# Performance work log

Hardware: AMD Instinct MI355X
Metric: run time of the kernel (lower is better)

## Reference

```python
import jax, jax.numpy as jnp
import numpy as np

NEG_SLOPE = 0.2

def gat_conv(x, src, dst, W, a_src, a_dst, bias, N):
    # PyG GATConv, heads=1: h = xW; e_ij = LeakyReLU(a_src.h_j + a_dst.h_i)
    h = x @ W                                   # [N, H]
    as_ = h @ a_src                             # [N]
    ad_ = h @ a_dst                             # [N]
    e = jax.nn.leaky_relu(as_[src] + ad_[dst], NEG_SLOPE)   # [E]
    m = jax.ops.segment_max(e, dst, num_segments=N)          # per-target max
    w = jnp.exp(e - m[dst])
    denom = jax.ops.segment_sum(w, dst, num_segments=N)
    alpha = w / (denom[dst] + 1e-16)                          # [E]
    out = jax.ops.segment_sum(alpha[:, None] * h[src], dst, num_segments=N)
    return out + bias


def setup_inputs() -> dict:
    key = jax.random.key(0)
    N, E, D, H, A = 20000, 320000, 256, 256, 8
    ks = jax.random.split(key, 16)
    s = lambda k, shp, fan: jax.random.normal(k, shp, jnp.float32) * (1.0 / np.sqrt(fan))
    return {
        "obs": jax.random.normal(ks[0], (N, D), jnp.float32),
        "edge_index": jax.random.randint(ks[1], (2, E), 0, N, dtype=jnp.int32),
        "W1": s(ks[2], (D, H), D), "a1_src": s(ks[3], (H,), H), "a1_dst": s(ks[4], (H,), H), "b1": jnp.zeros((H,), jnp.float32),
        "W2": s(ks[5], (H, H), H), "a2_src": s(ks[6], (H,), H), "a2_dst": s(ks[7], (H,), H), "b2": jnp.zeros((H,), jnp.float32),
        "Wm1": s(ks[8], (H, H), H), "bm1": jnp.zeros((H,), jnp.float32),
        "Wm2": s(ks[9], (H, A), H), "bm2": jnp.zeros((A,), jnp.float32),
    }


def reference(obs, edge_index, W1, a1_src, a1_dst, b1, W2, a2_src, a2_dst, b2, Wm1, bm1, Wm2, bm2):
    N = obs.shape[0]
    loops = jnp.arange(N, dtype=edge_index.dtype)
    src = jnp.concatenate([edge_index[0], loops])   # add self-loops (PyG default)
    dst = jnp.concatenate([edge_index[1], loops])
    x = jax.nn.relu(gat_conv(obs, src, dst, W1, a1_src, a1_dst, b1, N))
    x = jax.nn.relu(gat_conv(x,   src, dst, W2, a2_src, a2_dst, b2, N))
    x = jax.nn.relu(x @ Wm1 + bm1)
    return jnp.tanh(x @ Wm2 + bm2)
```

## Files before the change

kernel.cpp:

```cpp
#include <hip/hip_runtime.h>
#include <hip/hip_bf16.h>
#include <math.h>
#include <stdio.h>

typedef __attribute__((ext_vector_type(8))) short short8;
typedef __attribute__((ext_vector_type(4))) float f32x4;
typedef __attribute__((ext_vector_type(4))) unsigned short us4;

__device__ __forceinline__ float us2f(unsigned short u) {
    return __uint_as_float(((unsigned)u) << 16);
}
__device__ __forceinline__ unsigned short f2us_rtn(float f) {
    return (unsigned short)__bfloat16_as_ushort(__float2bfloat16(f));
}

__global__ void prep_all(const float* __restrict__ Wa, const float* __restrict__ Wb,
                         const float* __restrict__ Wc,
                         unsigned short* __restrict__ TA, unsigned short* __restrict__ TB,
                         unsigned short* __restrict__ TC,
                         const float* __restrict__ X, unsigned short* __restrict__ Xb,
                         float* __restrict__ as1, float* __restrict__ ad1,
                         float* __restrict__ as2, float* __restrict__ ad2,
                         int* __restrict__ deg,
                         int K, int Nn, int N, int tot8) {
    const int tot = K * Nn;
    int idx = blockIdx.x * blockDim.x + threadIdx.x;
    if (idx < 3 * tot) {
        const float* W;
        unsigned short* T;
        if (idx < tot) { W = Wa; T = TA; }
        else if (idx < 2 * tot) { W = Wb; T = TB; idx -= tot; }
        else { W = Wc; T = TC; idx -= 2 * tot; }
        const int n = idx / K, k = idx - n * K;
        T[idx] = f2us_rtn(W[(size_t)k * Nn + n]);
        return;
    }
    idx -= 3 * tot;
    if (idx < 5 * N) {
        if (idx < N) as1[idx] = 0.f;
        else if (idx < 2 * N) ad1[idx - N] = 0.f;
        else if (idx < 3 * N) as2[idx - 2 * N] = 0.f;
        else if (idx < 4 * N) ad2[idx - 3 * N] = 0.f;
        else deg[idx - 4 * N] = 0;
        return;
    }
    idx -= 5 * N;
    if (idx < tot8) {
        const float4 a = *(const float4*)(X + (size_t)idx * 8);
        const float4 b = *(const float4*)(X + (size_t)idx * 8 + 4);
        short8 o;
        const float f[8] = {a.x, a.y, a.z, a.w, b.x, b.y, b.z, b.w};
#pragma unroll
        for (int e = 0; e < 8; e++) o[e] = (short)f2us_rtn(f[e]);
        *(short8*)(Xb + (size_t)idx * 8) = o;
    }
}

#define LP 72
__global__ __launch_bounds__(256) void gemm_mfma(const unsigned short* __restrict__ A,
                                                 const unsigned short* __restrict__ Bt,
                                                 const float* __restrict__ avs,
                                                 const float* __restrict__ avd,
                                                 float* __restrict__ as_,
                                                 float* __restrict__ ad_,
                                                 unsigned short* __restrict__ C,
                                                 int M, int Nn, int K) {
    __shared__ unsigned short sA[64 * LP];
    __shared__ unsigned short sB[128 * LP];
    const int tid = threadIdx.x;
    const int wave = tid >> 6, lane = tid & 63;
    const int m16 = lane & 15, quad = lane >> 4;
    const int row0 = blockIdx.x * 64, col0 = blockIdx.y * 128;
    const int wr = (wave >> 1) * 32, wc = (wave & 1) * 64;
    const int ar = tid >> 2, akc = (tid & 3) * 8;
    const int bkc = (tid & 7) * 8, bcb = tid >> 3;

    f32x4 acc[2][4] = {};
    for (int k0 = 0; k0 < K; k0 += 64) {
        {
            const int gr = (row0 + ar) < M ? (row0 + ar) : (M - 1);
            const unsigned short* Ap = A + (size_t)gr * K + k0 + akc;
            *(short8*)&sA[ar * LP + akc]      = *(const short8*)Ap;
            *(short8*)&sA[ar * LP + akc + 32] = *(const short8*)(Ap + 32);
        }
#pragma unroll
        for (int q = 0; q < 4; q++) {
            const int colq = bcb + 32 * q;
            *(short8*)&sB[colq * LP + bkc] =
                *(const short8*)(Bt + (size_t)(col0 + colq) * K + k0 + bkc);
        }
        __syncthreads();
#pragma unroll
        for (int ks = 0; ks < 2; ks++) {
            short8 ah[2];
#pragma unroll
            for (int mi = 0; mi < 2; mi++)
                ah[mi] = *(const short8*)&sA[(wr + mi * 16 + m16) * LP + ks * 32 + quad * 8];
#pragma unroll
            for (int ni = 0; ni < 4; ni++) {
                const short8 bv = *(const short8*)&sB[(wc + ni * 16 + m16) * LP + ks * 32 + quad * 8];
#pragma unroll
                for (int mi = 0; mi < 2; mi++)
                    acc[mi][ni] = __builtin_amdgcn_mfma_f32_16x16x32_bf16(ah[mi], bv, acc[mi][ni], 0, 0, 0);
            }
        }
        __syncthreads();
    }
    float ps[2][4] = {}, pd[2][4] = {};
#pragma unroll
    for (int mi = 0; mi < 2; mi++) {
        const int orow_base = row0 + wr + mi * 16 + quad * 4;
#pragma unroll
        for (int ni = 0; ni < 4; ni++) {
            const int ocol = col0 + wc + ni * 16 + m16;
            const float asv = avs[ocol], adv = avd[ocol];
#pragma unroll
            for (int r = 0; r < 4; r++) {
                const int orow = orow_base + r;
                if (orow < M) {
                    const float v = acc[mi][ni][r];
                    C[(size_t)orow * Nn + ocol] = f2us_rtn(v);
                    ps[mi][r] = fmaf(v, asv, ps[mi][r]);
                    pd[mi][r] = fmaf(v, adv, pd[mi][r]);
                }
            }
        }
    }
#pragma unroll
    for (int mi = 0; mi < 2; mi++)
#pragma unroll
        for (int r = 0; r < 4; r++)
#pragma unroll
            for (int off = 1; off < 16; off <<= 1) {
                ps[mi][r] += __shfl_xor(ps[mi][r], off);
                pd[mi][r] += __shfl_xor(pd[mi][r], off);
            }
    if (m16 == 0) {
#pragma unroll
        for (int mi = 0; mi < 2; mi++) {
            const int orow_base = row0 + wr + mi * 16 + quad * 4;
#pragma unroll
            for (int r = 0; r < 4; r++) {
                const int orow = orow_base + r;
                if (orow < M) {
                    atomicAdd(&as_[orow], ps[mi][r]);
                    atomicAdd(&ad_[orow], pd[mi][r]);
                }
            }
        }
    }
}

__global__ __launch_bounds__(256) void gemm_head(const unsigned short* __restrict__ A,
                                                 const unsigned short* __restrict__ Bt,
                                                 const float* __restrict__ bias1,
                                                 const float* __restrict__ W2,
                                                 const float* __restrict__ bias2,
                                                 float* __restrict__ out,
                                                 int M, int K, int Aout) {
    __shared__ unsigned short sA[64 * LP];
    __shared__ unsigned short sB[256 * LP];
    __shared__ float pLDS[2][64][8];
    const int tid = threadIdx.x;
    const int wave = tid >> 6, lane = tid & 63;
    const int m16 = lane & 15, quad = lane >> 4;
    const int row0 = blockIdx.x * 64;
    const int wr = (wave >> 1) * 32, wc = (wave & 1) * 128;
    const int ar = tid >> 2, akc = (tid & 3) * 8;
    const int bkc = (tid & 7) * 8, bcb = tid >> 3;

    f32x4 acc[2][8] = {};
    for (int k0 = 0; k0 < K; k0 += 64) {
        {
            const int gr = (row0 + ar) < M ? (row0 + ar) : (M - 1);
            const unsigned short* Ap = A + (size_t)gr * K + k0 + akc;
            *(short8*)&sA[ar * LP + akc]      = *(const short8*)Ap;
            *(short8*)&sA[ar * LP + akc + 32] = *(const short8*)(Ap + 32);
        }
#pragma unroll
        for (int q = 0; q < 8; q++) {
            const int colq = bcb + 32 * q;
            *(short8*)&sB[colq * LP + bkc] =
                *(const short8*)(Bt + (size_t)colq * K + k0 + bkc);
        }
        __syncthreads();
#pragma unroll
        for (int ks = 0; ks < 2; ks++) {
            short8 ah[2];
#pragma unroll
            for (int mi = 0; mi < 2; mi++)
                ah[mi] = *(const short8*)&sA[(wr + mi * 16 + m16) * LP + ks * 32 + quad * 8];
#pragma unroll
            for (int ni = 0; ni < 8; ni++) {
                const short8 bv = *(const short8*)&sB[(wc + ni * 16 + m16) * LP + ks * 32 + quad * 8];
#pragma unroll
                for (int mi = 0; mi < 2; mi++)
                    acc[mi][ni] = __builtin_amdgcn_mfma_f32_16x16x32_bf16(ah[mi], bv, acc[mi][ni], 0, 0, 0);
            }
        }
        __syncthreads();
    }
    float p[2][4][8] = {};
#pragma unroll
    for (int ni = 0; ni < 8; ni++) {
        const int ocol = wc + ni * 16 + m16;
        const float b1v = bias1[ocol];
        float w2[8];
#pragma unroll
        for (int a = 0; a < 8; a++) w2[a] = W2[ocol * 8 + a];
#pragma unroll
        for (int mi = 0; mi < 2; mi++)
#pragma unroll
            for (int r = 0; r < 4; r++) {
                const float v = fmaxf(acc[mi][ni][r] + b1v, 0.f);
#pragma unroll
                for (int a = 0; a < 8; a++) p[mi][r][a] = fmaf(v, w2[a], p[mi][r][a]);
            }
    }
#pragma unroll
    for (int off = 1; off < 16; off <<= 1)
#pragma unroll
        for (int mi = 0; mi < 2; mi++)
#pragma unroll
            for (int r = 0; r < 4; r++)
#pragma unroll
                for (int a = 0; a < 8; a++) p[mi][r][a] += __shfl_xor(p[mi][r][a], off);
    if (m16 == 0) {
        const int half = wc >> 7;
#pragma unroll
        for (int mi = 0; mi < 2; mi++) {
            const int lrow = wr + mi * 16 + quad * 4;
#pragma unroll
            for (int r = 0; r < 4; r++)
#pragma unroll
                for (int a = 0; a < 8; a++) pLDS[half][lrow + r][a] = p[mi][r][a];
        }
    }
    __syncthreads();
#pragma unroll
    for (int u = 0; u < 2; u++) {
        const int idx = tid * 2 + u;
        const int lrow = idx >> 3, a = idx & 7;
        const int orow = row0 + lrow;
        if (orow < M && a < Aout)
            out[(size_t)orow * Aout + a] =
                tanhf(pLDS[0][lrow][a] + pLDS[1][lrow][a] + bias2[a]);
    }
}
#undef LP

__global__ void count_kernel(const int* __restrict__ dstA, int* __restrict__ deg, int E, int Etot) {
    const int e = blockIdx.x * blockDim.x + threadIdx.x;
    if (e >= Etot) return;
    const int d = (e < E) ? dstA[e] : (e - E);
    atomicAdd(&deg[d], 1);
}

__global__ __launch_bounds__(1024) void scan_kernel(const int* __restrict__ deg,
                                                    int* __restrict__ offs,
                                                    int* __restrict__ cursor, int N) {
    __shared__ int sums[1024];
    const int t = threadIdx.x;
    const int chunk = (N + 1023) / 1024;
    const int start = t * chunk;
    int s = 0;
    for (int i = 0; i < chunk; i++) {
        const int p = start + i;
        if (p < N) s += deg[p];
    }
    sums[t] = s;
    __syncthreads();
    for (int off = 1; off < 1024; off <<= 1) {
        const int add = (t >= off) ? sums[t - off] : 0;
        __syncthreads();
        sums[t] += add;
        __syncthreads();
    }
    int run = (t > 0) ? sums[t - 1] : 0;
    for (int i = 0; i < chunk; i++) {
        const int p = start + i;
        if (p < N) { offs[p] = run; cursor[p] = run; run += deg[p]; }
    }
    if (t == 0) offs[N] = sums[1023];
}

__global__ void scatter_kernel(const int* __restrict__ srcA, const int* __restrict__ dstA,
                               int* __restrict__ cursor, int* __restrict__ esrc, int E, int Etot) {
    const int e = blockIdx.x * blockDim.x + threadIdx.x;
    if (e >= Etot) return;
    int s, d;
    if (e < E) { s = srcA[e]; d = dstA[e]; } else { s = d = e - E; }
    const int slot = atomicAdd(&cursor[d], 1);
    esrc[slot] = s;
}

__global__ __launch_bounds__(256) void agg_kernel(const unsigned short* __restrict__ hb,
                                                  const int* __restrict__ offs,
                                                  const int* __restrict__ esrc,
                                                  const float* __restrict__ as_,
                                                  const float* __restrict__ ad_,
                                                  const float* __restrict__ bias,
                                                  unsigned short* __restrict__ xout, int N) {
    const int n = blockIdx.x * 4 + (threadIdx.x >> 6);
    if (n >= N) return;
    const int lane = threadIdx.x & 63;
    const int f0 = lane * 4;
    const int b = offs[n], e2 = offs[n + 1];
    const float adn = ad_[n];
    float a0 = 0.f, a1 = 0.f, a2 = 0.f, a3 = 0.f, wsum = 0.f;
    int j = b;
    for (; j + 8 <= e2; j += 8) {
        int s[8];
#pragma unroll
        for (int u = 0; u < 8; u++) s[u] = esrc[j + u];
        us4 pv[8];
#pragma unroll
        for (int u = 0; u < 8; u++) pv[u] = *(const us4*)(hb + (size_t)s[u] * 256 + f0);
        float w[8];
#pragma unroll
        for (int u = 0; u < 8; u++) {
            float v = as_[s[u]] + adn;
            v = v > 0.f ? v : 0.2f * v;
            w[u] = __expf(v);
        }
#pragma unroll
        for (int u = 0; u < 8; u++) {
            a0 = fmaf(w[u], us2f(pv[u][0]), a0);
            a1 = fmaf(w[u], us2f(pv[u][1]), a1);
            a2 = fmaf(w[u], us2f(pv[u][2]), a2);
            a3 = fmaf(w[u], us2f(pv[u][3]), a3);
            wsum += w[u];
        }
    }
    for (; j < e2; j++) {
        const int s = esrc[j];
        float v = as_[s] + adn;
        v = v > 0.f ? v : 0.2f * v;
        const float w = __expf(v);
        const us4 pv = *(const us4*)(hb + (size_t)s * 256 + f0);
        a0 = fmaf(w, us2f(pv[0]), a0);
        a1 = fmaf(w, us2f(pv[1]), a1);
        a2 = fmaf(w, us2f(pv[2]), a2);
        a3 = fmaf(w, us2f(pv[3]), a3);
        wsum += w;
    }
    const float inv = 1.0f / (wsum + 1e-16f);
    float r0 = fmaxf(a0 * inv + bias[f0], 0.f);
    float r1 = fmaxf(a1 * inv + bias[f0 + 1], 0.f);
    float r2 = fmaxf(a2 * inv + bias[f0 + 2], 0.f);
    float r3 = fmaxf(a3 * inv + bias[f0 + 3], 0.f);
    us4 o;
    o[0] = f2us_rtn(r0); o[1] = f2us_rtn(r1); o[2] = f2us_rtn(r2); o[3] = f2us_rtn(r3);
    *(us4*)(xout + (size_t)n * 256 + f0) = o;
}

extern "C" void kernel_launch(void* const* d_in, const int* in_sizes, int n_in,
                              void* d_out, int out_size, void* d_ws, size_t ws_size,
                              hipStream_t stream) {
    const float* obs = (const float*)d_in[0];
    const int* eidx  = (const int*)d_in[1];
    const float* W1  = (const float*)d_in[2];
    const float* a1s = (const float*)d_in[3];
    const float* a1d = (const float*)d_in[4];
    const float* b1  = (const float*)d_in[5];
    const float* W2  = (const float*)d_in[6];
    const float* a2s = (const float*)d_in[7];
    const float* a2d = (const float*)d_in[8];
    const float* b2v = (const float*)d_in[9];
    const float* Wm1 = (const float*)d_in[10];
    const float* bm1 = (const float*)d_in[11];
    const float* Wm2 = (const float*)d_in[12];
    const float* bm2 = (const float*)d_in[13];
    float* out = (float*)d_out;

    const int Hh = in_sizes[3];
    const int Dd = in_sizes[2] / Hh;
    const int N  = in_sizes[0] / Dd;
    const int E  = in_sizes[1] / 2;
    const int Etot = E + N;
    const int Aout = in_sizes[12] / Hh;

    const int* srcA = eidx;
    const int* dstA = eidx + E;

    size_t off = 0;
    char* ws = (char*)d_ws;
    auto alloc = [&](size_t bytes) -> char* {
        char* p = ws + off;
        off = (off + bytes + 15) & ~(size_t)15;
        return p;
    };
    unsigned short* obs_b = (unsigned short*)alloc((size_t)N * Dd * 2);
    unsigned short* h     = (unsigned short*)alloc((size_t)N * Hh * 2);
    unsigned short* xb    = (unsigned short*)alloc((size_t)N * Hh * 2);
    float* as1   = (float*)alloc((size_t)N * 4);
    float* ad1   = (float*)alloc((size_t)N * 4);
    float* as2   = (float*)alloc((size_t)N * 4);
    float* ad2   = (float*)alloc((size_t)N * 4);
    int* deg     = (int*)alloc((size_t)N * 4);
    int* offs    = (int*)alloc((size_t)(N + 1) * 4);
    int* cursor  = (int*)alloc((size_t)N * 4);
    int* esrc    = (int*)alloc((size_t)Etot * 4);
    const size_t wsz = (size_t)Dd * Hh;
    unsigned short* W1t = (unsigned short*)alloc(wsz * 2);
    unsigned short* W2t = (unsigned short*)alloc(wsz * 2);
    unsigned short* Wmt = (unsigned short*)alloc(wsz * 2);

    const int eb = 256;
    const int eg = (Etot + eb - 1) / eb;
    const dim3 ggrid((N + 63) / 64, Hh / 128);
    const int nrow = (N + 63) / 64;

    const int tot8 = (N * Dd) / 8;
    const int ptot = 3 * (int)wsz + 5 * N + tot8;
    prep_all<<<(ptot + 255) / 256, 256, 0, stream>>>(
        W1, W2, Wm1, W1t, W2t, Wmt, obs, obs_b, as1, ad1, as2, ad2, deg, Dd, Hh, N, tot8);

    count_kernel<<<eg, eb, 0, stream>>>(dstA, deg, E, Etot);
    scan_kernel<<<1, 1024, 0, stream>>>(deg, offs, cursor, N);
    scatter_kernel<<<eg, eb, 0, stream>>>(srcA, dstA, cursor, esrc, E, Etot);

    gemm_mfma<<<ggrid, 256, 0, stream>>>(obs_b, W1t, a1s, a1d, as1, ad1, h, N, Hh, Dd);
    agg_kernel<<<(N + 3) / 4, 256, 0, stream>>>(h, offs, esrc, as1, ad1, b1, xb, N);

    gemm_mfma<<<ggrid, 256, 0, stream>>>(xb, W2t, a2s, a2d, as2, ad2, h, N, Hh, Hh);
    agg_kernel<<<(N + 3) / 4, 256, 0, stream>>>(h, offs, esrc, as2, ad2, b2v, xb, N);

    gemm_head<<<nrow, 256, 0, stream>>>(xb, Wmt, bm1, Wm2, bm2, out, N, Hh, Aout);
}
```

Measured before the change: 266.0 us.

## Fuse fp32-to-bf16 obs conversion into GEMM load and split aggregation by feature slice

The first GEMM now reads fp32 obs directly and converts it to bf16 while staging into shared memory. This removes the separate conversion pass in prep_all and the bf16 copy of obs it wrote to the workspace. The aggregation kernel is also split so that each block handles one 64-feature slice of four nodes, with each lane reading a single bf16 element instead of four. That gives four times more blocks for parallelism, but recomputes the edge weights four times and issues narrower gathers.

```diff
diff --git a/kernel.cpp b/kernel.cpp
--- a/kernel.cpp
+++ b/kernel.cpp
@@ -14,15 +14,27 @@
     return (unsigned short)__bfloat16_as_ushort(__float2bfloat16(f));
 }
 
+__device__ __forceinline__ void stage8(const unsigned short* Ap, unsigned short* dst) {
+    *(short8*)dst = *(const short8*)Ap;
+}
+__device__ __forceinline__ void stage8(const float* Ap, unsigned short* dst) {
+    const float4 a = *(const float4*)Ap;
+    const float4 b = *(const float4*)(Ap + 4);
+    const float f[8] = {a.x, a.y, a.z, a.w, b.x, b.y, b.z, b.w};
+    short8 o;
+#pragma unroll
+    for (int e = 0; e < 8; e++) o[e] = (short)f2us_rtn(f[e]);
+    *(short8*)dst = o;
+}
+
 __global__ void prep_all(const float* __restrict__ Wa, const float* __restrict__ Wb,
                          const float* __restrict__ Wc,
                          unsigned short* __restrict__ TA, unsigned short* __restrict__ TB,
                          unsigned short* __restrict__ TC,
-                         const float* __restrict__ X, unsigned short* __restrict__ Xb,
                          float* __restrict__ as1, float* __restrict__ ad1,
                          float* __restrict__ as2, float* __restrict__ ad2,
                          int* __restrict__ deg,
-                         int K, int Nn, int N, int tot8) {
+                         int K, int Nn, int N) {
     const int tot = K * Nn;
     int idx = blockIdx.x * blockDim.x + threadIdx.x;
     if (idx < 3 * tot) {
@@ -42,22 +54,12 @@
         else if (idx < 3 * N) as2[idx - 2 * N] = 0.f;
         else if (idx < 4 * N) ad2[idx - 3 * N] = 0.f;
         else deg[idx - 4 * N] = 0;
-        return;
-    }
-    idx -= 5 * N;
-    if (idx < tot8) {
-        const float4 a = *(const float4*)(X + (size_t)idx * 8);
-        const float4 b = *(const float4*)(X + (size_t)idx * 8 + 4);
-        short8 o;
-        const float f[8] = {a.x, a.y, a.z, a.w, b.x, b.y, b.z, b.w};
-#pragma unroll
-        for (int e = 0; e < 8; e++) o[e] = (short)f2us_rtn(f[e]);
-        *(short8*)(Xb + (size_t)idx * 8) = o;
     }
 }
 
 #define LP 72
-__global__ __launch_bounds__(256) void gemm_mfma(const unsigned short* __restrict__ A,
+template <typename TA>
+__global__ __launch_bounds__(256) void gemm_mfma(const TA* __restrict__ A,
                                                  const unsigned short* __restrict__ Bt,
                                                  const float* __restrict__ avs,
                                                  const float* __restrict__ avd,
@@ -79,9 +81,9 @@
     for (int k0 = 0; k0 < K; k0 += 64) {
         {
             const int gr = (row0 + ar) < M ? (row0 + ar) : (M - 1);
-            const unsigned short* Ap = A + (size_t)gr * K + k0 + akc;
-            *(short8*)&sA[ar * LP + akc]      = *(const short8*)Ap;
-            *(short8*)&sA[ar * LP + akc + 32] = *(const short8*)(Ap + 32);
+            const TA* Ap = A + (size_t)gr * K + k0 + akc;
+            stage8(Ap,      &sA[ar * LP + akc]);
+            stage8(Ap + 32, &sA[ar * LP + akc + 32]);
         }
 #pragma unroll
         for (int q = 0; q < 4; q++) {
@@ -301,21 +303,22 @@
                                                   const float* __restrict__ ad_,
                                                   const float* __restrict__ bias,
                                                   unsigned short* __restrict__ xout, int N) {
-    const int n = blockIdx.x * 4 + (threadIdx.x >> 6);
+    const int bI = blockIdx.x;
+    const int slice = bI & 3;
+    const int n = (bI >> 2) * 4 + (threadIdx.x >> 6);
     if (n >= N) return;
-    const int lane = threadIdx.x & 63;
-    const int f0 = lane * 4;
+    const int f = slice * 64 + (threadIdx.x & 63);
     const int b = offs[n], e2 = offs[n + 1];
     const float adn = ad_[n];
-    float a0 = 0.f, a1 = 0.f, a2 = 0.f, a3 = 0.f, wsum = 0.f;
+    float acc = 0.f, wsum = 0.f;
     int j = b;
     for (; j + 8 <= e2; j += 8) {
         int s[8];
 #pragma unroll
         for (int u = 0; u < 8; u++) s[u] = esrc[j + u];
-        us4 pv[8];
-#pragma unroll
-        for (int u = 0; u < 8; u++) pv[u] = *(const us4*)(hb + (size_t)s[u] * 256 + f0);
+        float hv[8];
+#pragma unroll
+        for (int u = 0; u < 8; u++) hv[u] = us2f(hb[(size_t)s[u] * 256 + f]);
         float w[8];
 #pragma unroll
         for (int u = 0; u < 8; u++) {
@@ -324,34 +327,18 @@
             w[u] = __expf(v);
         }
 #pragma unroll
-        for (int u = 0; u < 8; u++) {
-            a0 = fmaf(w[u], us2f(pv[u][0]), a0);
-            a1 = fmaf(w[u], us2f(pv[u][1]), a1);
-            a2 = fmaf(w[u], us2f(pv[u][2]), a2);
-            a3 = fmaf(w[u], us2f(pv[u][3]), a3);
-            wsum += w[u];
-        }
+        for (int u = 0; u < 8; u++) { acc = fmaf(w[u], hv[u], acc); wsum += w[u]; }
     }
     for (; j < e2; j++) {
         const int s = esrc[j];
         float v = as_[s] + adn;
         v = v > 0.f ? v : 0.2f * v;
         const float w = __expf(v);
-        const us4 pv = *(const us4*)(hb + (size_t)s * 256 + f0);
-        a0 = fmaf(w, us2f(pv[0]), a0);
-        a1 = fmaf(w, us2f(pv[1]), a1);
-        a2 = fmaf(w, us2f(pv[2]), a2);
-        a3 = fmaf(w, us2f(pv[3]), a3);
+        acc = fmaf(w, us2f(hb[(size_t)s * 256 + f]), acc);
         wsum += w;
     }
-    const float inv = 1.0f / (wsum + 1e-16f);
-    float r0 = fmaxf(a0 * inv + bias[f0], 0.f);
-    float r1 = fmaxf(a1 * inv + bias[f0 + 1], 0.f);
-    float r2 = fmaxf(a2 * inv + bias[f0 + 2], 0.f);
-    float r3 = fmaxf(a3 * inv + bias[f0 + 3], 0.f);
-    us4 o;
-    o[0] = f2us_rtn(r0); o[1] = f2us_rtn(r1); o[2] = f2us_rtn(r2); o[3] = f2us_rtn(r3);
-    *(us4*)(xout + (size_t)n * 256 + f0) = o;
+    const float r = fmaxf(acc / (wsum + 1e-16f) + bias[f], 0.f);
+    xout[(size_t)n * 256 + f] = f2us_rtn(r);
 }
 
 extern "C" void kernel_launch(void* const* d_in, const int* in_sizes, int n_in,
@@ -390,9 +377,8 @@
         off = (off + bytes + 15) & ~(size_t)15;
         return p;
     };
-    unsigned short* obs_b = (unsigned short*)alloc((size_t)N * Dd * 2);
-    unsigned short* h     = (unsigned short*)alloc((size_t)N * Hh * 2);
-    unsigned short* xb    = (unsigned short*)alloc((size_t)N * Hh * 2);
+    unsigned short* h  = (unsigned short*)alloc((size_t)N * Hh * 2);
+    unsigned short* xb = (unsigned short*)alloc((size_t)N * Hh * 2);
     float* as1   = (float*)alloc((size_t)N * 4);
     float* ad1   = (float*)alloc((size_t)N * 4);
     float* as2   = (float*)alloc((size_t)N * 4);
@@ -410,21 +396,21 @@
     const int eg = (Etot + eb - 1) / eb;
     const dim3 ggrid((N + 63) / 64, Hh / 128);
     const int nrow = (N + 63) / 64;
-
-    const int tot8 = (N * Dd) / 8;
-    const int ptot = 3 * (int)wsz + 5 * N + tot8;
+    const int agrid = ((N + 3) / 4) * 4;
+
+    const int ptot = 3 * (int)wsz + 5 * N;
     prep_all<<<(ptot + 255) / 256, 256, 0, stream>>>(
-        W1, W2, Wm1, W1t, W2t, Wmt, obs, obs_b, as1, ad1, as2, ad2, deg, Dd, Hh, N, tot8);
+        W1, W2, Wm1, W1t, W2t, Wmt, as1, ad1, as2, ad2, deg, Dd, Hh, N);
 
     count_kernel<<<eg, eb, 0, stream>>>(dstA, deg, E, Etot);
     scan_kernel<<<1, 1024, 0, stream>>>(deg, offs, cursor, N);
     scatter_kernel<<<eg, eb, 0, stream>>>(srcA, dstA, cursor, esrc, E, Etot);
 
-    gemm_mfma<<<ggrid, 256, 0, stream>>>(obs_b, W1t, a1s, a1d, as1, ad1, h, N, Hh, Dd);
-    agg_kernel<<<(N + 3) / 4, 256, 0, stream>>>(h, offs, esrc, as1, ad1, b1, xb, N);
-
-    gemm_mfma<<<ggrid, 256, 0, stream>>>(xb, W2t, a2s, a2d, as2, ad2, h, N, Hh, Hh);
-    agg_kernel<<<(N + 3) / 4, 256, 0, stream>>>(h, offs, esrc, as2, ad2, b2v, xb, N);
+    gemm_mfma<float><<<ggrid, 256, 0, stream>>>(obs, W1t, a1s, a1d, as1, ad1, h, N, Hh, Dd);
+    agg_kernel<<<agrid, 256, 0, stream>>>(h, offs, esrc, as1, ad1, b1, xb, N);
+
+    gemm_mfma<unsigned short><<<ggrid, 256, 0, stream>>>(xb, W2t, a2s, a2d, as2, ad2, h, N, Hh, Hh);
+    agg_kernel<<<agrid, 256, 0, stream>>>(h, offs, esrc, as2, ad2, b2v, xb, N);
 
     gemm_head<<<nrow, 256, 0, stream>>>(xb, Wmt, bm1, Wm2, bm2, out, N, Hh, Aout);
 }
```

After: 321.7 us. +21.0%, slower.
